# Optimization experiments

Measured on AMD Instinct MI355X. Metric: run time of the kernel, lower is better.

The kernel has to match this reference:

```python
import jax, jax.numpy as jnp
import numpy as np

HEADS = 4
TOKEN_CH = 128
D_HEAD = TOKEN_CH // HEADS  # 32


def setup_inputs() -> dict:
    key = jax.random.key(0)
    ks = jax.random.split(key, 12)
    B, QC, Z, H, W = 4, 256, 16, 32, 32
    N, KVC = 256, 512
    s = lambda k, shape, fan: jax.random.normal(k, shape, jnp.float32) * (1.0 / np.sqrt(fan))
    return {
        "feat":   jax.random.normal(ks[0], (B, QC, Z, H, W), jnp.float32),
        "tokens": jax.random.normal(ks[1], (B, N, KVC), jnp.float32),
        "qw":   s(ks[2], (TOKEN_CH, QC), QC),      # Conv3d 1x1 -> [out, in]
        "qb":   jnp.zeros((TOKEN_CH,), jnp.float32),
        "kw":   s(ks[3], (TOKEN_CH, KVC), KVC),    # Linear, no bias
        "vw":   s(ks[4], (TOKEN_CH, KVC), KVC),
        "projw": s(ks[5], (QC, TOKEN_CH), TOKEN_CH),
        "projb": jnp.zeros((QC,), jnp.float32),
        "ff1w": s(ks[6], (QC * 2, QC), QC),
        "ff1b": jnp.zeros((QC * 2,), jnp.float32),
        "ff2w": s(ks[7], (QC, QC * 2), QC * 2),
        "ff2b": jnp.zeros((QC,), jnp.float32),
        "gate": jnp.zeros((1,), jnp.float32),
    }


def _conv1x1(x, w, b):
    # x: [B, Cin, Z, H, W], w: [Cout, Cin] -> [B, Cout, Z, H, W]
    return jnp.einsum('bczhw,oc->bozhw', x, w) + b[None, :, None, None, None]


def reference(feat, tokens, qw, qb, kw, vw, projw, projb, ff1w, ff1b, ff2w, ff2b, gate):
    B, C, Z, H, W = feat.shape
    S = Z * H * W
    scale = D_HEAD ** (-0.5)

    # Q: conv1x1 then split heads -> [B, nh, S, dh]
    q = _conv1x1(feat, qw, qb).reshape(B, HEADS, D_HEAD, S).transpose(0, 1, 3, 2)
    # K, V: linear (no bias) -> [B, nh, N, dh]
    k = jnp.einsum('bnc,tc->bnt', tokens, kw).reshape(B, -1, HEADS, D_HEAD).transpose(0, 2, 1, 3)
    v = jnp.einsum('bnc,tc->bnt', tokens, vw).reshape(B, -1, HEADS, D_HEAD).transpose(0, 2, 1, 3)

    attn = jax.nn.softmax(jnp.einsum('bhsd,bhnd->bhsn', q, k) * scale, axis=-1)
    out = jnp.einsum('bhsn,bhnd->bhsd', attn, v)  # [B, nh, S, dh]

    # merge heads back to channel-first volume: b (nh dh) z h w
    out = out.transpose(0, 1, 3, 2).reshape(B, TOKEN_CH, Z, H, W)
    out = _conv1x1(out, projw, projb)

    out = feat + jnp.tanh(gate[0]) * out
    ff = _conv1x1(jax.nn.silu(_conv1x1(out, ff1w, ff1b)), ff2w, ff2b)
    return out + ff
```

## Files before the change

### kernel.cpp

```cpp
#include <hip/hip_runtime.h>

#define NB 4
#define QC 256
#define SD 16384
#define NT 256
#define KVC 512
#define TC 128
#define NH 4
#define DH 32
#define TSP 64
#define XPITCH 260
#define HPITCH 132

typedef unsigned short u16;
typedef __attribute__((ext_vector_type(8))) short bf16x8;
typedef __attribute__((ext_vector_type(4))) short bf16x4;
typedef __attribute__((ext_vector_type(4))) float f32x4;

union ABFrag { bf16x4 h[2]; bf16x8 v; };

__device__ __forceinline__ float b2f(u16 u) {
  unsigned int v = ((unsigned int)u) << 16;
  return __builtin_bit_cast(float, v);
}
__device__ __forceinline__ u16 f2b(float f) {
  unsigned int x = __builtin_bit_cast(unsigned int, f);
  unsigned int r = (x + 0x7fffu + ((x >> 16) & 1u)) >> 16;
  return (u16)r;
}

__global__ __launch_bounds__(256) void pack_kernel(
    const float* __restrict__ ff1w, const float* __restrict__ ff2w,
    u16* __restrict__ w1p, u16* __restrict__ w2p) {
  int idx = blockIdx.x * 256 + threadIdx.x;
  int lane = idx & 63;
  int m = lane & 15, q = lane >> 4;
  if (idx < 16384) {
    int kblk = (idx >> 6) & 7;
    int jblk = idx >> 9;
    const float* src = ff1w + (size_t)(jblk * 16 + m) * QC + kblk * 32 + q * 8;
    u16* dst = w1p + (size_t)idx * 8;
#pragma unroll
    for (int i = 0; i < 8; i++) dst[i] = f2b(src[i]);
  } else {
    int s2 = idx - 16384;
    int kblk = (s2 >> 6) & 15;
    int oblk = s2 >> 10;
    const float* src = ff2w + (size_t)(oblk * 16 + m) * KVC + kblk * 32 + q * 8;
    u16* dst = w2p + (size_t)s2 * 8;
#pragma unroll
    for (int i = 0; i < 8; i++) dst[i] = f2b(src[i]);
  }
}

__global__ __launch_bounds__(256) void kv_kernel(
    const float* __restrict__ tokens, const float* __restrict__ kw,
    const float* __restrict__ vw, const float* __restrict__ gate,
    float* __restrict__ ws_kv) {
  float tg = tanhf(gate[0]);
  if (tg == 0.0f) return;
  int b = blockIdx.x >> 8;
  int n = blockIdx.x & 255;
  __shared__ float tok[KVC];
  for (int c = threadIdx.x; c < KVC; c += 256)
    tok[c] = tokens[((size_t)(b * NT + n)) * KVC + c];
  __syncthreads();
  int tid = threadIdx.x;
  int t = tid & 127;
  const float* w = (tid < 128) ? kw : vw;
  const float* wr = w + (size_t)t * KVC;
  float acc = 0.f;
  for (int c = 0; c < KVC; c += 4) {
    float4 wv = *(const float4*)(wr + c);
    acc += tok[c] * wv.x + tok[c + 1] * wv.y + tok[c + 2] * wv.z + tok[c + 3] * wv.w;
  }
  int h = t >> 5, d = t & 31;
  float* dst = ws_kv + ((tid < 128) ? 0 : NB * NH * NT * DH);
  dst[(((b * NH + h) * NT) + n) * DH + d] = acc;
}

__global__ __launch_bounds__(256, 2) void fused_kernel(
    const float* __restrict__ feat, const float* __restrict__ qw,
    const float* __restrict__ qb, const float* __restrict__ projw,
    const float* __restrict__ projb, const float* __restrict__ ff1b,
    const float* __restrict__ ff2b, const u16* __restrict__ w1p,
    const u16* __restrict__ w2p, const float* __restrict__ gate,
    const float* __restrict__ ws_kv, float* __restrict__ out) {
  __shared__ u16 sX[TSP * XPITCH];
  __shared__ u16 sH[TSP * HPITCH];

  int b = blockIdx.x >> 8;
  int s0 = (blockIdx.x & 255) * TSP;
  int tid = threadIdx.x;
  int w = tid >> 6;
  int lane = tid & 63;
  int lm = lane & 15, lq = lane >> 4;

  {
    const float* fb = feat + (((size_t)b * QC) << 14) + s0 + lane;
#pragma unroll
    for (int it = 0; it < 16; ++it) {
      int c0 = it * 16 + w * 4;
      const float* gp = fb + ((size_t)c0 << 14);
      ushort4 pk;
      pk.x = f2b(gp[0]);
      pk.y = f2b(gp[16384]);
      pk.z = f2b(gp[32768]);
      pk.w = f2b(gp[49152]);
      *(ushort4*)&sX[lane * XPITCH + c0] = pk;
    }
  }
  float tg = tanhf(gate[0]);
  __syncthreads();

  if (tg != 0.0f) {
    float qreg[DH];
#pragma unroll
    for (int d = 0; d < DH; d++) {
      int o = w * DH + d;
      float a = qb[o];
      const float* qr = qw + (size_t)o * QC;
      for (int c = 0; c < QC; c += 4) {
        float4 wv = *(const float4*)(qr + c);
        a += b2f(sX[lane * XPITCH + c + 0]) * wv.x;
        a += b2f(sX[lane * XPITCH + c + 1]) * wv.y;
        a += b2f(sX[lane * XPITCH + c + 2]) * wv.z;
        a += b2f(sX[lane * XPITCH + c + 3]) * wv.w;
      }
      qreg[d] = a;
    }
    const float* Kp = ws_kv + (size_t)(b * NH + w) * NT * DH;
    const float* Vp = Kp + NB * NH * NT * DH;
    float m_ = -1e30f, l_ = 0.f;
    float oacc[DH];
#pragma unroll
    for (int d = 0; d < DH; d++) oacc[d] = 0.f;
    const float scale = 0.17677669529663687f;
    for (int n = 0; n < NT; n++) {
      const float* kr = Kp + n * DH;
      float s = 0.f;
#pragma unroll
      for (int d = 0; d < DH; d++) s += qreg[d] * kr[d];
      s *= scale;
      float nm = fmaxf(m_, s);
      float p = __expf(s - nm);
      float al = __expf(m_ - nm);
      const float* vr = Vp + n * DH;
      l_ = l_ * al + p;
#pragma unroll
      for (int d = 0; d < DH; d++) oacc[d] = oacc[d] * al + p * vr[d];
      m_ = nm;
    }
    float inv = 1.0f / l_;
#pragma unroll
    for (int d = 0; d < DH; d++)
      sH[lane * HPITCH + w * DH + d] = f2b(oacc[d] * inv);
    __syncthreads();
    for (int ci = 0; ci < 64; ci++) {
      int c = w * 64 + ci;
      float a = projb[c];
      const float* pr = projw + (size_t)c * TC;
      for (int t = 0; t < TC; t += 4) {
        float4 wv = *(const float4*)(pr + t);
        a += b2f(sH[lane * HPITCH + t + 0]) * wv.x;
        a += b2f(sH[lane * HPITCH + t + 1]) * wv.y;
        a += b2f(sH[lane * HPITCH + t + 2]) * wv.z;
        a += b2f(sH[lane * HPITCH + t + 3]) * wv.w;
      }
      float o1 = b2f(sX[lane * XPITCH + c]) + tg * a;
      sX[lane * XPITCH + c] = f2b(o1);
    }
    __syncthreads();
  }

  const f32x4 fzero = {0.f, 0.f, 0.f, 0.f};
  f32x4 acc2[4][4];
#pragma unroll
  for (int t = 0; t < 4; t++)
#pragma unroll
    for (int m = 0; m < 4; m++) acc2[t][m] = fzero;

#pragma unroll 1
  for (int ch = 0; ch < 4; ++ch) {
    f32x4 acc1[2][4];
#pragma unroll
    for (int t = 0; t < 2; t++)
#pragma unroll
      for (int m = 0; m < 4; m++) acc1[t][m] = fzero;
#pragma unroll 2
    for (int k = 0; k < 8; ++k) {
      ABFrag a[4];
      int col = k * 32 + lq * 8;
#pragma unroll
      for (int m = 0; m < 4; m++) {
        int row = m * 16 + lm;
        a[m].h[0] = *(const bf16x4*)&sX[row * XPITCH + col];
        a[m].h[1] = *(const bf16x4*)&sX[row * XPITCH + col + 4];
      }
#pragma unroll
      for (int t = 0; t < 2; t++) {
        int jblk = ch * 8 + w * 2 + t;
        bf16x8 bf = *(const bf16x8*)(w1p + (((size_t)jblk * 8 + k) * 64 + lane) * 8);
#pragma unroll
        for (int m = 0; m < 4; m++)
          acc1[t][m] = __builtin_amdgcn_mfma_f32_16x16x32_bf16(a[m].v, bf, acc1[t][m], 0, 0, 0);
      }
    }
    __syncthreads();
#pragma unroll
    for (int t = 0; t < 2; t++) {
      int jl = (w * 2 + t) * 16 + lm;
      float b1 = ff1b[ch * 128 + jl];
#pragma unroll
      for (int m = 0; m < 4; m++) {
        int sb = m * 16 + lq * 4;
        f32x4 v = acc1[t][m];
#pragma unroll
        for (int r = 0; r < 4; r++) {
          float x = v[r] + b1;
          float sl = x / (1.f + __expf(-x));
          sH[(sb + r) * HPITCH + jl] = f2b(sl);
        }
      }
    }
    __syncthreads();
#pragma unroll 2
    for (int k = 0; k < 4; ++k) {
      ABFrag a[4];
      int col = k * 32 + lq * 8;
#pragma unroll
      for (int m = 0; m < 4; m++) {
        int row = m * 16 + lm;
        a[m].h[0] = *(const bf16x4*)&sH[row * HPITCH + col];
        a[m].h[1] = *(const bf16x4*)&sH[row * HPITCH + col + 4];
      }
      int kg = ch * 4 + k;
#pragma unroll
      for (int t = 0; t < 4; t++) {
        int oblk = w * 4 + t;
        bf16x8 bf = *(const bf16x8*)(w2p + (((size_t)oblk * 16 + kg) * 64 + lane) * 8);
#pragma unroll
        for (int m = 0; m < 4; m++)
          acc2[t][m] = __builtin_amdgcn_mfma_f32_16x16x32_bf16(a[m].v, bf, acc2[t][m], 0, 0, 0);
      }
    }
  }

#pragma unroll
  for (int t = 0; t < 4; t++) {
    int c = (w * 4 + t) * 16 + lm;
    float bias = ff2b[c];
#pragma unroll
    for (int m = 0; m < 4; m++) {
      int sb = m * 16 + lq * 4;
      f32x4 v = acc2[t][m];
      float4 ov;
      ov.x = v[0] + bias + b2f(sX[(sb + 0) * XPITCH + c]);
      ov.y = v[1] + bias + b2f(sX[(sb + 1) * XPITCH + c]);
      ov.z = v[2] + bias + b2f(sX[(sb + 2) * XPITCH + c]);
      ov.w = v[3] + bias + b2f(sX[(sb + 3) * XPITCH + c]);
      *(float4*)(out + (((size_t)(b * QC + c)) << 14) + s0 + sb) = ov;
    }
  }
}

extern "C" void kernel_launch(void* const* d_in, const int* in_sizes, int n_in,
                              void* d_out, int out_size, void* d_ws, size_t ws_size,
                              hipStream_t stream) {
  const float* feat   = (const float*)d_in[0];
  const float* tokens = (const float*)d_in[1];
  const float* qw     = (const float*)d_in[2];
  const float* qb     = (const float*)d_in[3];
  const float* kw     = (const float*)d_in[4];
  const float* vw     = (const float*)d_in[5];
  const float* projw  = (const float*)d_in[6];
  const float* projb  = (const float*)d_in[7];
  const float* ff1w   = (const float*)d_in[8];
  const float* ff1b   = (const float*)d_in[9];
  const float* ff2w   = (const float*)d_in[10];
  const float* ff2b   = (const float*)d_in[11];
  const float* gate   = (const float*)d_in[12];
  float* out = (float*)d_out;

  u16* w1p = (u16*)d_ws;
  u16* w2p = w1p + 131072;
  float* ws_kv = (float*)((char*)d_ws + 524288);

  pack_kernel<<<dim3(128), dim3(256), 0, stream>>>(ff1w, ff2w, w1p, w2p);
  kv_kernel<<<dim3(NB * NT), dim3(256), 0, stream>>>(tokens, kw, vw, gate, ws_kv);
  fused_kernel<<<dim3(NB * (SD / TSP)), dim3(256), 0, stream>>>(
      feat, qw, qb, projw, projb, ff1b, ff2b, w1p, w2p, gate, ws_kv, out);
}
```

Before: 204.8 us.

## Prefetch MFMA weight fragments, vectorize feat staging, raise occupancy hint

Raises launch_bounds min blocks from 2 to 3 per CU. Rewrites the feat-to-LDS staging so each thread reads a float4 along the spatial axis instead of four scalar strided loads. Fully unrolls both FF GEMM k-loops and software-prefetches the next k-step's bf16 weight fragments from global memory while the current MFMAs run, to hide global load latency. This costs extra registers, which may conflict with the higher occupancy target and cause spills, and the transposed scalar LDS stores may bank-conflict.

```diff
diff --git a/kernel.cpp b/kernel.cpp
--- a/kernel.cpp
+++ b/kernel.cpp
@@ -79,7 +79,7 @@
   dst[(((b * NH + h) * NT) + n) * DH + d] = acc;
 }
 
-__global__ __launch_bounds__(256, 2) void fused_kernel(
+__global__ __launch_bounds__(256, 3) void fused_kernel(
     const float* __restrict__ feat, const float* __restrict__ qw,
     const float* __restrict__ qb, const float* __restrict__ projw,
     const float* __restrict__ projb, const float* __restrict__ ff1b,
@@ -97,17 +97,17 @@
   int lm = lane & 15, lq = lane >> 4;
 
   {
-    const float* fb = feat + (((size_t)b * QC) << 14) + s0 + lane;
+    const float* fb = feat + (((size_t)b * QC) << 14) + s0;
+    int cst = tid >> 4;
+    int ss = (tid & 15) * 4;
 #pragma unroll
     for (int it = 0; it < 16; ++it) {
-      int c0 = it * 16 + w * 4;
-      const float* gp = fb + ((size_t)c0 << 14);
-      ushort4 pk;
-      pk.x = f2b(gp[0]);
-      pk.y = f2b(gp[16384]);
-      pk.z = f2b(gp[32768]);
-      pk.w = f2b(gp[49152]);
-      *(ushort4*)&sX[lane * XPITCH + c0] = pk;
+      int c = it * 16 + cst;
+      float4 v = *(const float4*)(fb + ((size_t)c << 14) + ss);
+      sX[(ss + 0) * XPITCH + c] = f2b(v.x);
+      sX[(ss + 1) * XPITCH + c] = f2b(v.y);
+      sX[(ss + 2) * XPITCH + c] = f2b(v.z);
+      sX[(ss + 3) * XPITCH + c] = f2b(v.w);
     }
   }
   float tg = tanhf(gate[0]);
@@ -187,61 +187,89 @@
     for (int t = 0; t < 2; t++)
 #pragma unroll
       for (int m = 0; m < 4; m++) acc1[t][m] = fzero;
-#pragma unroll 2
-    for (int k = 0; k < 8; ++k) {
-      ABFrag a[4];
-      int col = k * 32 + lq * 8;
-#pragma unroll
-      for (int m = 0; m < 4; m++) {
-        int row = m * 16 + lm;
-        a[m].h[0] = *(const bf16x4*)&sX[row * XPITCH + col];
-        a[m].h[1] = *(const bf16x4*)&sX[row * XPITCH + col + 4];
-      }
-#pragma unroll
-      for (int t = 0; t < 2; t++) {
-        int jblk = ch * 8 + w * 2 + t;
-        bf16x8 bf = *(const bf16x8*)(w1p + (((size_t)jblk * 8 + k) * 64 + lane) * 8);
+
+    {
+      int jb0 = ch * 8 + w * 2;
+      const u16* bp0 = w1p + ((size_t)(jb0 + 0) * 8 * 64 + lane) * 8;
+      const u16* bp1 = w1p + ((size_t)(jb0 + 1) * 8 * 64 + lane) * 8;
+      bf16x8 b0 = *(const bf16x8*)bp0;
+      bf16x8 b1 = *(const bf16x8*)bp1;
+#pragma unroll
+      for (int k = 0; k < 8; ++k) {
+        ABFrag a[4];
+        int col = k * 32 + lq * 8;
+#pragma unroll
+        for (int m = 0; m < 4; m++) {
+          int row = m * 16 + lm;
+          a[m].h[0] = *(const bf16x4*)&sX[row * XPITCH + col];
+          a[m].h[1] = *(const bf16x4*)&sX[row * XPITCH + col + 4];
+        }
+        bf16x8 n0, n1;
+        if (k < 7) {
+          n0 = *(const bf16x8*)(bp0 + (size_t)(k + 1) * 64 * 8);
+          n1 = *(const bf16x8*)(bp1 + (size_t)(k + 1) * 64 * 8);
+        }
 #pragma unroll
         for (int m = 0; m < 4; m++)
-          acc1[t][m] = __builtin_amdgcn_mfma_f32_16x16x32_bf16(a[m].v, bf, acc1[t][m], 0, 0, 0);
+          acc1[0][m] = __builtin_amdgcn_mfma_f32_16x16x32_bf16(a[m].v, b0, acc1[0][m], 0, 0, 0);
+#pragma unroll
+        for (int m = 0; m < 4; m++)
+          acc1[1][m] = __builtin_amdgcn_mfma_f32_16x16x32_bf16(a[m].v, b1, acc1[1][m], 0, 0, 0);
+        if (k < 7) { b0 = n0; b1 = n1; }
       }
     }
     __syncthreads();
 #pragma unroll
     for (int t = 0; t < 2; t++) {
       int jl = (w * 2 + t) * 16 + lm;
-      float b1 = ff1b[ch * 128 + jl];
+      float b1v = ff1b[ch * 128 + jl];
 #pragma unroll
       for (int m = 0; m < 4; m++) {
         int sb = m * 16 + lq * 4;
         f32x4 v = acc1[t][m];
 #pragma unroll
         for (int r = 0; r < 4; r++) {
-          float x = v[r] + b1;
+          float x = v[r] + b1v;
           float sl = x / (1.f + __expf(-x));
           sH[(sb + r) * HPITCH + jl] = f2b(sl);
         }
       }
     }
     __syncthreads();
-#pragma unroll 2
-    for (int k = 0; k < 4; ++k) {
-      ABFrag a[4];
-      int col = k * 32 + lq * 8;
-#pragma unroll
-      for (int m = 0; m < 4; m++) {
-        int row = m * 16 + lm;
-        a[m].h[0] = *(const bf16x4*)&sH[row * HPITCH + col];
-        a[m].h[1] = *(const bf16x4*)&sH[row * HPITCH + col + 4];
-      }
-      int kg = ch * 4 + k;
+    {
+      const u16* bp[4];
+      bf16x8 bb[4];
 #pragma unroll
       for (int t = 0; t < 4; t++) {
         int oblk = w * 4 + t;
-        bf16x8 bf = *(const bf16x8*)(w2p + (((size_t)oblk * 16 + kg) * 64 + lane) * 8);
-#pragma unroll
-        for (int m = 0; m < 4; m++)
-          acc2[t][m] = __builtin_amdgcn_mfma_f32_16x16x32_bf16(a[m].v, bf, acc2[t][m], 0, 0, 0);
+        bp[t] = w2p + ((size_t)(oblk * 16 + ch * 4) * 64 + lane) * 8;
+        bb[t] = *(const bf16x8*)bp[t];
+      }
+#pragma unroll
+      for (int k = 0; k < 4; ++k) {
+        ABFrag a[4];
+        int col = k * 32 + lq * 8;
+#pragma unroll
+        for (int m = 0; m < 4; m++) {
+          int row = m * 16 + lm;
+          a[m].h[0] = *(const bf16x4*)&sH[row * HPITCH + col];
+          a[m].h[1] = *(const bf16x4*)&sH[row * HPITCH + col + 4];
+        }
+        bf16x8 nb[4];
+        if (k < 3) {
+#pragma unroll
+          for (int t = 0; t < 4; t++)
+            nb[t] = *(const bf16x8*)(bp[t] + (size_t)(k + 1) * 64 * 8);
+        }
+#pragma unroll
+        for (int t = 0; t < 4; t++)
+#pragma unroll
+          for (int m = 0; m < 4; m++)
+            acc2[t][m] = __builtin_amdgcn_mfma_f32_16x16x32_bf16(a[m].v, bb[t], acc2[t][m], 0, 0, 0);
+        if (k < 3) {
+#pragma unroll
+          for (int t = 0; t < 4; t++) bb[t] = nb[t];
+        }
       }
     }
   }
```

After: 199.3 us. -2.7%, faster.
